# Performance work log

Measured on AMD Instinct MI355X. Metric: run time of the kernel, lower is better.

Reference implementation:

```python
import jax, jax.numpy as jnp
import numpy as np

D_MODEL = 1024
NUM_HEADS = 16
D_K = D_MODEL // NUM_HEADS


def setup_inputs() -> dict:
    key = jax.random.key(0)
    ks = jax.random.split(key, 9)
    B, S = 4, 2048
    scale = 1.0 / np.sqrt(D_MODEL)
    x = jax.random.normal(ks[0], (B, S, D_MODEL), dtype=jnp.float32)
    Wq = jax.random.uniform(ks[1], (D_MODEL, D_MODEL), jnp.float32, -scale, scale)
    Wk = jax.random.uniform(ks[2], (D_MODEL, D_MODEL), jnp.float32, -scale, scale)
    Wv = jax.random.uniform(ks[3], (D_MODEL, D_MODEL), jnp.float32, -scale, scale)
    Wo = jax.random.uniform(ks[4], (D_MODEL, D_MODEL), jnp.float32, -scale, scale)
    bq = jax.random.uniform(ks[5], (D_MODEL,), jnp.float32, -scale, scale)
    bk = jax.random.uniform(ks[6], (D_MODEL,), jnp.float32, -scale, scale)
    bv = jax.random.uniform(ks[7], (D_MODEL,), jnp.float32, -scale, scale)
    bo = jax.random.uniform(ks[8], (D_MODEL,), jnp.float32, -scale, scale)
    return {"x": x, "Wq": Wq, "bq": bq, "Wk": Wk, "bk": bk, "Wv": Wv, "bv": bv, "Wo": Wo, "bo": bo}


def _split_heads(t, B, S):
    # (B, S, D) -> (B, H, S, d_k)
    return t.reshape(B, S, NUM_HEADS, D_K).transpose(0, 2, 1, 3)


def reference(x, Wq, bq, Wk, bk, Wv, bv, Wo, bo):
    B, S, D = x.shape
    Q = _split_heads(x @ Wq + bq, B, S)
    K = _split_heads(x @ Wk + bk, B, S)
    V = _split_heads(x @ Wv + bv, B, S)
    # scores: (B, H, S, S) — naive materialization, faithful to original
    scores = jnp.einsum('bhqd,bhkd->bhqk', Q, K) / np.sqrt(D_K)
    weights = jax.nn.softmax(scores.astype(jnp.float32), axis=-1).astype(scores.dtype)
    # dropout p=0.0 in eval mode -> identity
    attn = jnp.einsum('bhqk,bhkd->bhqd', weights, V)
    attn = attn.transpose(0, 2, 1, 3).reshape(B, S, D)
    return attn @ Wo + bo
```

## Files before the change

kernel.cpp:

```cpp
#include <hip/hip_runtime.h>
#include <hip/hip_bf16.h>
#include <stdint.h>
#include <string.h>

using u16 = unsigned short;
typedef __attribute__((ext_vector_type(8))) short short8;
typedef __attribute__((ext_vector_type(4))) float f32x4;

__device__ __forceinline__ u16 f2bf(float f) {
  union { float f; unsigned int u; } x; x.f = f;
  unsigned int u = x.u;
  return (u16)((u + 0x7fffu + ((u >> 16) & 1u)) >> 16);
}
__device__ __forceinline__ unsigned int pk_bf16(float a, float b) {
  float2 t; t.x = a; t.y = b;
  __hip_bfloat162 h = __float22bfloat162_rn(t);
  unsigned int u; memcpy(&u, &h, 4);
  return u;
}
__device__ __forceinline__ void gl_lds16(const u16* g, u16* l) {
  __builtin_amdgcn_global_load_lds((const __attribute__((address_space(1))) void*)g,
                                   (__attribute__((address_space(3))) void*)l, 16, 0, 0);
}

__device__ __forceinline__ void pl_swap(unsigned int& a, unsigned int& b) {
  auto r1 = __builtin_amdgcn_permlane32_swap(a, b, false, false);
  auto r2 = __builtin_amdgcn_permlane16_swap(r1[0], r1[1], false, false);
  a = r2[0]; b = r2[1];
}

#define SCALE_LOG2E 0.18033688011112042f

__global__ void __launch_bounds__(256) conv_x(
    const float* __restrict__ in, u16* __restrict__ out, int n4) {
  const int t = blockIdx.x * 256 + threadIdx.x;
  if (t >= n4) return;
  const float4 v = ((const float4*)in)[t];
  uint2 o;
  o.x = pk_bf16(v.x, v.y);
  o.y = pk_bf16(v.z, v.w);
  ((uint2*)out)[t] = o;
}

__global__ void __launch_bounds__(256) transpose_w(
    const float* __restrict__ W0, const float* __restrict__ W1,
    const float* __restrict__ W2, const float* __restrict__ W3,
    u16* __restrict__ Wt) {
  __shared__ alignas(16) u16 t[64][65];
  const int z = blockIdx.z;
  const float* in = (z == 0) ? W0 : (z == 1) ? W1 : (z == 2) ? W2 : W3;
  u16* out = Wt + (size_t)z * 1024 * 1024;
  const int tx = threadIdx.x & 63, ty = threadIdx.x >> 6;
  const int r0 = blockIdx.y * 64, c0 = blockIdx.x * 64;
#pragma unroll
  for (int rr = ty; rr < 64; rr += 4) t[rr][tx] = f2bf(in[(size_t)(r0 + rr) * 1024 + c0 + tx]);
  __syncthreads();
#pragma unroll
  for (int rr = ty; rr < 64; rr += 4) out[(size_t)(c0 + rr) * 1024 + r0 + tx] = t[tx][rr];
}

__device__ __forceinline__ void gemm_core(
    const u16* __restrict__ A, const u16* __restrict__ Bt,
    u16* As, u16* Bs, int m0, int n0, int K, f32x4 (&acc)[4][4]) {
  const int tid = threadIdx.x;
  const int wave = tid >> 6, lane = tid & 63;
  const int quad = lane >> 4, l16 = lane & 15;
  const int wr = wave >> 1, wc = wave & 1;
  const int lr = lane >> 2, lc = (lane & 3) * 8;
  for (int k0 = 0; k0 < K; k0 += 32) {
    __syncthreads();
#pragma unroll
    for (int t = 0; t < 2; ++t) {
      const int c = wave + t * 4;
      gl_lds16(A  + (size_t)(m0 + c * 16 + lr) * K + k0 + lc, &As[c * 16 * 32]);
      gl_lds16(Bt + (size_t)(n0 + c * 16 + lr) * K + k0 + lc, &Bs[c * 16 * 32]);
    }
    __syncthreads();
    short8 af[4], bfr[4];
#pragma unroll
    for (int i = 0; i < 4; ++i)
      af[i] = *(const short8*)&As[(wr * 64 + i * 16 + l16) * 32 + quad * 8];
#pragma unroll
    for (int j = 0; j < 4; ++j)
      bfr[j] = *(const short8*)&Bs[(wc * 64 + j * 16 + l16) * 32 + quad * 8];
#pragma unroll
    for (int i = 0; i < 4; ++i)
#pragma unroll
      for (int j = 0; j < 4; ++j)
        acc[i][j] = __builtin_amdgcn_mfma_f32_16x16x32_bf16(af[i], bfr[j], acc[i][j], 0, 0, 0);
  }
}

__global__ void __launch_bounds__(256) gemm_qkv(
    const u16* __restrict__ A, const u16* __restrict__ Wt,
    const float* __restrict__ bq, const float* __restrict__ bk, const float* __restrict__ bv,
    u16* __restrict__ Qb, u16* __restrict__ Kb, u16* __restrict__ Vtb) {
  __shared__ alignas(16) u16 As[128 * 32];
  __shared__ alignas(16) u16 Bs[128 * 32];
  const int tsel = blockIdx.x >> 3;
  const int n0 = (blockIdx.x & 7) * 128;
  const int m0 = blockIdx.y * 128;
  const u16* Bt = Wt + (size_t)tsel * 1048576;
  const float* bias = (tsel == 0) ? bq : (tsel == 1) ? bk : bv;

  f32x4 acc[4][4];
#pragma unroll
  for (int i = 0; i < 4; ++i)
#pragma unroll
    for (int j = 0; j < 4; ++j) acc[i][j] = (f32x4){0.f, 0.f, 0.f, 0.f};

  gemm_core(A, Bt, As, Bs, m0, n0, 1024, acc);

  const int tid = threadIdx.x;
  const int wave = tid >> 6, lane = tid & 63;
  const int quad = lane >> 4, l16 = lane & 15;
  const int wr = wave >> 1, wc = wave & 1;

  if (tsel < 2) {
    u16* C = tsel ? Kb : Qb;
    const float scl = tsel ? 1.0f : SCALE_LOG2E;
#pragma unroll
    for (int j = 0; j < 4; ++j) {
      const int n = n0 + wc * 64 + j * 16 + l16;
      const float bvf = bias[n];
      const int h = n >> 6, d = n & 63;
#pragma unroll
      for (int i = 0; i < 4; ++i) {
        const int mbase = m0 + wr * 64 + i * 16 + quad * 4;
#pragma unroll
        for (int r = 0; r < 4; ++r) {
          const int m = mbase + r;
          const int b = m >> 11, s = m & 2047;
          C[((((size_t)b * 16 + h) * 2048) + s) * 64 + d] = f2bf((acc[i][j][r] + bvf) * scl);
        }
      }
    }
  } else {
#pragma unroll
    for (int j = 0; j < 4; ++j) {
      const int n = n0 + wc * 64 + j * 16 + l16;
      const float bvf = bias[n];
      const int h = n >> 6, d = n & 63;
#pragma unroll
      for (int i = 0; i < 4; ++i) {
        const int mbase = m0 + wr * 64 + i * 16 + quad * 4;
        const int b = mbase >> 11, s = mbase & 2047;
        uint2 o;
        o.x = pk_bf16(acc[i][j][0] + bvf, acc[i][j][1] + bvf);
        o.y = pk_bf16(acc[i][j][2] + bvf, acc[i][j][3] + bvf);
        *(uint2*)&Vtb[(((size_t)b * 16 + h) * 64 + d) * 2048 + s] = o;
      }
    }
  }
}

__global__ void __launch_bounds__(256) gemm_out(
    const u16* __restrict__ A, const u16* __restrict__ Bt,
    const float* __restrict__ bias, float* __restrict__ C, int N) {
  __shared__ alignas(16) u16 As[128 * 32];
  __shared__ alignas(16) u16 Bs[128 * 32];
  const int m0 = blockIdx.y * 128;
  const int n0 = blockIdx.x * 128;
  f32x4 acc[4][4];
#pragma unroll
  for (int i = 0; i < 4; ++i)
#pragma unroll
    for (int j = 0; j < 4; ++j) acc[i][j] = (f32x4){0.f, 0.f, 0.f, 0.f};

  gemm_core(A, Bt, As, Bs, m0, n0, 1024, acc);

  const int tid = threadIdx.x;
  const int wave = tid >> 6, lane = tid & 63;
  const int quad = lane >> 4, l16 = lane & 15;
  const int wr = wave >> 1, wc = wave & 1;
#pragma unroll
  for (int j = 0; j < 4; ++j) {
    const int n = n0 + wc * 64 + j * 16 + l16;
    const float bvf = bias[n];
#pragma unroll
    for (int i = 0; i < 4; ++i) {
      const int mbase = m0 + wr * 64 + i * 16 + quad * 4;
#pragma unroll
      for (int r = 0; r < 4; ++r)
        C[(size_t)(mbase + r) * N + n] = acc[i][j][r] + bvf;
    }
  }
}

__global__ void __launch_bounds__(256) flash_attn(
    const u16* __restrict__ Q, const u16* __restrict__ Kp,
    const u16* __restrict__ Vt, u16* __restrict__ Aout) {
  __shared__ alignas(16) u16 Qs[128 * 64];
  __shared__ alignas(16) u16 Ks[2][64 * 64];
  __shared__ alignas(16) u16 Vs[2][64 * 64];

  const int tid = threadIdx.x;
  const int wave = tid >> 6;
  const int lane = tid & 63;
  const int quad = lane >> 4;
  const int l16 = lane & 15;

  const int i = blockIdx.x;
  const int bh = (i & 7) * 8 + (i >> 7);
  const int q0 = ((i >> 3) & 15) * 128;
  const int b = bh >> 4, h = bh & 15;

  const u16* Qg = Q + (size_t)bh * 2048 * 64;
  const u16* Kg = Kp + (size_t)bh * 2048 * 64;
  const u16* Vg = Vt + (size_t)bh * 64 * 2048;

  const int lr8 = lane >> 3;
  const int cbg = ((lane & 7) ^ lr8) * 8;

#pragma unroll
  for (int t = 0; t < 4; ++t) {
    const int c = wave * 4 + t;
    gl_lds16(Qg + (size_t)(q0 + c * 8 + lr8) * 64 + cbg, &Qs[c * 8 * 64]);
  }
  {
#pragma unroll
    for (int t = 0; t < 2; ++t) {
      const int c = wave * 2 + t;
      gl_lds16(Kg + (size_t)(c * 8 + lr8) * 64 + cbg, &Ks[0][c * 8 * 64]);
      gl_lds16(Vg + (size_t)(c * 8 + lr8) * 2048 + cbg, &Vs[0][c * 8 * 64]);
    }
  }

  f32x4 oacc[2][4];
#pragma unroll
  for (int qb = 0; qb < 2; ++qb)
#pragma unroll
    for (int t = 0; t < 4; ++t) oacc[qb][t] = (f32x4){0.f, 0.f, 0.f, 0.f};
  f32x4 lacc[2];
  lacc[0] = (f32x4){0.f, 0.f, 0.f, 0.f};
  lacc[1] = (f32x4){0.f, 0.f, 0.f, 0.f};
  const int sw = (l16 & 7) * 8;

  short8 ones;
#pragma unroll
  for (int i2 = 0; i2 < 8; ++i2) ones[i2] = (short)0x3F80;

  __syncthreads();
  short8 qf[2][2];
#pragma unroll
  for (int qb = 0; qb < 2; ++qb)
#pragma unroll
    for (int ks = 0; ks < 2; ++ks)
      qf[qb][ks] = *(const short8*)&Qs[(wave * 32 + qb * 16 + l16) * 64 + (((ks * 4 + quad) * 8) ^ sw)];

  for (int kt = 0; kt < 32; ++kt) {
    const int p = kt & 1;
    if (kt + 1 < 32) {
      const int s1 = (kt + 1) * 64;
#pragma unroll
      for (int t = 0; t < 2; ++t) {
        const int c = wave * 2 + t;
        gl_lds16(Kg + (size_t)(s1 + c * 8 + lr8) * 64 + cbg, &Ks[p ^ 1][c * 8 * 64]);
        gl_lds16(Vg + (size_t)(c * 8 + lr8) * 2048 + s1 + cbg, &Vs[p ^ 1][c * 8 * 64]);
      }
    }
    const u16* Kc = &Ks[p][0];
    const u16* Vc = &Vs[p][0];

    f32x4 sacc[2][4];
#pragma unroll
    for (int qb = 0; qb < 2; ++qb)
#pragma unroll
      for (int t = 0; t < 4; ++t) sacc[qb][t] = (f32x4){0.f, 0.f, 0.f, 0.f};
#pragma unroll
    for (int ks = 0; ks < 2; ++ks) {
#pragma unroll
      for (int t = 0; t < 4; ++t) {
        const short8 akf = *(const short8*)&Kc[(t * 16 + l16) * 64 + (((ks * 4 + quad) * 8) ^ sw)];
#pragma unroll
        for (int qb = 0; qb < 2; ++qb)
          sacc[qb][t] = __builtin_amdgcn_mfma_f32_16x16x32_bf16(akf, qf[qb][ks], sacc[qb][t], 0, 0, 0);
      }
    }

    short8 bpf[2][2];
#pragma unroll
    for (int qb = 0; qb < 2; ++qb) {
      unsigned int w[4][2];
#pragma unroll
      for (int t = 0; t < 4; ++t) {
        const float p0 = __builtin_amdgcn_exp2f(sacc[qb][t][0]);
        const float p1 = __builtin_amdgcn_exp2f(sacc[qb][t][1]);
        const float p2 = __builtin_amdgcn_exp2f(sacc[qb][t][2]);
        const float p3 = __builtin_amdgcn_exp2f(sacc[qb][t][3]);
        w[t][0] = pk_bf16(p0, p1);
        w[t][1] = pk_bf16(p2, p3);
      }
      pl_swap(w[0][0], w[1][0]);
      pl_swap(w[0][1], w[1][1]);
      pl_swap(w[2][0], w[3][0]);
      pl_swap(w[2][1], w[3][1]);
      union { short8 s8; unsigned int u[4]; } pb;
      pb.u[0] = w[0][0]; pb.u[1] = w[0][1]; pb.u[2] = w[1][0]; pb.u[3] = w[1][1];
      bpf[qb][0] = pb.s8;
      pb.u[0] = w[2][0]; pb.u[1] = w[2][1]; pb.u[2] = w[3][0]; pb.u[3] = w[3][1];
      bpf[qb][1] = pb.s8;
    }

#pragma unroll
    for (int s = 0; s < 2; ++s)
#pragma unroll
      for (int qb = 0; qb < 2; ++qb)
        lacc[qb] = __builtin_amdgcn_mfma_f32_16x16x32_bf16(ones, bpf[qb][s], lacc[qb], 0, 0, 0);

#pragma unroll
    for (int s = 0; s < 2; ++s) {
#pragma unroll
      for (int t = 0; t < 4; ++t) {
        const short8 avf = *(const short8*)&Vc[(t * 16 + l16) * 64 + (((s * 4 + quad) * 8) ^ sw)];
#pragma unroll
        for (int qb = 0; qb < 2; ++qb)
          oacc[qb][t] = __builtin_amdgcn_mfma_f32_16x16x32_bf16(avf, bpf[qb][s], oacc[qb][t], 0, 0, 0);
      }
    }

    __syncthreads();
  }

#pragma unroll
  for (int qb = 0; qb < 2; ++qb) {
    const float inv = 1.0f / lacc[qb][0];
    const int qrow = q0 + wave * 32 + qb * 16 + l16;
    const size_t base = ((size_t)b * 2048 + qrow) * 1024 + h * 64 + quad * 4;
#pragma unroll
    for (int t = 0; t < 4; ++t) {
      uint2 o;
      o.x = pk_bf16(oacc[qb][t][0] * inv, oacc[qb][t][1] * inv);
      o.y = pk_bf16(oacc[qb][t][2] * inv, oacc[qb][t][3] * inv);
      *(uint2*)&Aout[base + t * 16] = o;
    }
  }
}

extern "C" void kernel_launch(void* const* d_in, const int* in_sizes, int n_in,
                              void* d_out, int out_size, void* d_ws, size_t ws_size,
                              hipStream_t stream) {
  (void)in_sizes; (void)n_in; (void)out_size; (void)ws_size;
  const float* x  = (const float*)d_in[0];
  const float* Wq = (const float*)d_in[1];
  const float* bq = (const float*)d_in[2];
  const float* Wk = (const float*)d_in[3];
  const float* bk = (const float*)d_in[4];
  const float* Wv = (const float*)d_in[5];
  const float* bv = (const float*)d_in[6];
  const float* Wo = (const float*)d_in[7];
  const float* bo = (const float*)d_in[8];
  float* out = (float*)d_out;

  u16* ws = (u16*)d_ws;
  const size_t SZ = (size_t)4 * 16 * 2048 * 64;
  u16* xb   = ws;
  u16* Qb   = ws + SZ;
  u16* Kb   = ws + 2 * SZ;
  u16* Vtb  = ws + 3 * SZ;
  u16* Wt   = ws + 4 * SZ;
  u16* Attn = ws;

  dim3 blk(256);
  conv_x<<<dim3(8192), blk, 0, stream>>>(x, xb, 2097152);
  transpose_w<<<dim3(16, 16, 4), blk, 0, stream>>>(Wq, Wk, Wv, Wo, Wt);
  gemm_qkv<<<dim3(24, 64), blk, 0, stream>>>(xb, Wt, bq, bk, bv, Qb, Kb, Vtb);
  flash_attn<<<dim3(1024), blk, 0, stream>>>(Qb, Kb, Vtb, Attn);
  gemm_out<<<dim3(8, 64), blk, 0, stream>>>(Attn, Wt + (size_t)3 * 1048576, bo, out, 1024);
}
```

Before: 316.0 us.

## Rewrite projection GEMMs as 256x128 tiles with double-buffered swizzled LDS pipeline

Replaces the simple 128x128, K=32 GEMM core with a 256x128 tile per 512-thread block. It uses K=64 steps, XOR-swizzled LDS layout and double-buffered global-to-LDS loads that are staggered across two MFMA phases, plus s_setprio around the MFMA bursts. The aim is to hide global load latency, avoid LDS bank conflicts and raise data reuse per block. The cost is higher LDS use (96KB per block), more register pressure and fewer blocks (768 and 256), which may underfill the GPU.

```diff
diff --git a/kernel.cpp b/kernel.cpp
--- a/kernel.cpp
+++ b/kernel.cpp
@@ -59,47 +59,114 @@
   for (int rr = ty; rr < 64; rr += 4) out[(size_t)(c0 + rr) * 1024 + r0 + tx] = t[tx][rr];
 }
 
-__device__ __forceinline__ void gemm_core(
+__device__ __forceinline__ void gemm256_core(
     const u16* __restrict__ A, const u16* __restrict__ Bt,
-    u16* As, u16* Bs, int m0, int n0, int K, f32x4 (&acc)[4][4]) {
+    u16 (*As)[16384], u16 (*Bs)[8192],
+    int m0, int n0, int K, f32x4 (&acc)[4][4]) {
   const int tid = threadIdx.x;
   const int wave = tid >> 6, lane = tid & 63;
   const int quad = lane >> 4, l16 = lane & 15;
-  const int wr = wave >> 1, wc = wave & 1;
-  const int lr = lane >> 2, lc = (lane & 3) * 8;
-  for (int k0 = 0; k0 < K; k0 += 32) {
-    __syncthreads();
-#pragma unroll
-    for (int t = 0; t < 2; ++t) {
-      const int c = wave + t * 4;
-      gl_lds16(A  + (size_t)(m0 + c * 16 + lr) * K + k0 + lc, &As[c * 16 * 32]);
-      gl_lds16(Bt + (size_t)(n0 + c * 16 + lr) * K + k0 + lc, &Bs[c * 16 * 32]);
-    }
-    __syncthreads();
-    short8 af[4], bfr[4];
+  const int wm = wave >> 1, wn = wave & 1;
+  const int lr8 = lane >> 3;
+  const int cbg = ((lane & 7) ^ lr8) * 8;
+  const int NT = K >> 6;
+
+  const int arow = wm * 64 + l16;
+  const int brow = wn * 64 + l16;
+  int kx[2];
+  kx[0] = ((quad    ) ^ (l16 & 7)) * 8;
+  kx[1] = ((quad + 4) ^ (l16 & 7)) * 8;
+
+#pragma unroll
+  for (int u = 0; u < 4; ++u)
+    gl_lds16(A + (size_t)(m0 + u * 64 + wave * 8 + lr8) * K + cbg,
+             &As[0][u * 4096 + wave * 512]);
+#pragma unroll
+  for (int v = 0; v < 2; ++v)
+    gl_lds16(Bt + (size_t)(n0 + v * 64 + wave * 8 + lr8) * K + cbg,
+             &Bs[0][v * 4096 + wave * 512]);
+#pragma unroll
+  for (int u = 0; u < 3; ++u)
+    gl_lds16(A + (size_t)(m0 + u * 64 + wave * 8 + lr8) * K + 64 + cbg,
+             &As[1][u * 4096 + wave * 512]);
+  asm volatile("s_waitcnt vmcnt(3)" ::: "memory");
+  __builtin_amdgcn_s_barrier();
+
+  for (int t = 0; t < NT; ++t) {
+    const int p = t & 1;
+    const u16* Ap = As[p];
+    const u16* Bp = Bs[p];
+
+    short8 af[4][2], bf[2][2];
 #pragma unroll
     for (int i = 0; i < 4; ++i)
-      af[i] = *(const short8*)&As[(wr * 64 + i * 16 + l16) * 32 + quad * 8];
-#pragma unroll
-    for (int j = 0; j < 4; ++j)
-      bfr[j] = *(const short8*)&Bs[(wc * 64 + j * 16 + l16) * 32 + quad * 8];
-#pragma unroll
-    for (int i = 0; i < 4; ++i)
-#pragma unroll
-      for (int j = 0; j < 4; ++j)
-        acc[i][j] = __builtin_amdgcn_mfma_f32_16x16x32_bf16(af[i], bfr[j], acc[i][j], 0, 0, 0);
-  }
-}
-
-__global__ void __launch_bounds__(256) gemm_qkv(
+#pragma unroll
+      for (int ks = 0; ks < 2; ++ks)
+        af[i][ks] = *(const short8*)&Ap[(arow + i * 16) * 64 + kx[ks]];
+#pragma unroll
+    for (int j = 0; j < 2; ++j)
+#pragma unroll
+      for (int ks = 0; ks < 2; ++ks)
+        bf[j][ks] = *(const short8*)&Bp[(brow + j * 16) * 64 + kx[ks]];
+    if (t + 1 < NT) {
+      gl_lds16(A + (size_t)(m0 + 3 * 64 + wave * 8 + lr8) * K + (t + 1) * 64 + cbg,
+               &As[p ^ 1][3 * 4096 + wave * 512]);
+      gl_lds16(Bt + (size_t)(n0 + wave * 8 + lr8) * K + (t + 1) * 64 + cbg,
+               &Bs[p ^ 1][wave * 512]);
+      gl_lds16(Bt + (size_t)(n0 + 64 + wave * 8 + lr8) * K + (t + 1) * 64 + cbg,
+               &Bs[p ^ 1][4096 + wave * 512]);
+    }
+    __builtin_amdgcn_s_barrier();
+    __builtin_amdgcn_s_setprio(1);
+#pragma unroll
+    for (int ks = 0; ks < 2; ++ks)
+#pragma unroll
+      for (int i = 0; i < 4; ++i)
+#pragma unroll
+        for (int j = 0; j < 2; ++j)
+          acc[i][j] = __builtin_amdgcn_mfma_f32_16x16x32_bf16(af[i][ks], bf[j][ks], acc[i][j], 0, 0, 0);
+    __builtin_amdgcn_s_setprio(0);
+    __builtin_amdgcn_s_barrier();
+
+#pragma unroll
+    for (int j = 0; j < 2; ++j)
+#pragma unroll
+      for (int ks = 0; ks < 2; ++ks)
+        bf[j][ks] = *(const short8*)&Bp[(brow + (j + 2) * 16) * 64 + kx[ks]];
+    if (t + 2 < NT) {
+#pragma unroll
+      for (int u = 0; u < 3; ++u)
+        gl_lds16(A + (size_t)(m0 + u * 64 + wave * 8 + lr8) * K + (t + 2) * 64 + cbg,
+                 &As[p][u * 4096 + wave * 512]);
+    }
+    __builtin_amdgcn_s_barrier();
+    __builtin_amdgcn_s_setprio(1);
+#pragma unroll
+    for (int ks = 0; ks < 2; ++ks)
+#pragma unroll
+      for (int i = 0; i < 4; ++i)
+#pragma unroll
+        for (int j = 0; j < 2; ++j)
+          acc[i][j + 2] = __builtin_amdgcn_mfma_f32_16x16x32_bf16(af[i][ks], bf[j][ks], acc[i][j + 2], 0, 0, 0);
+    __builtin_amdgcn_s_setprio(0);
+    if (t + 2 < NT) {
+      asm volatile("s_waitcnt vmcnt(3)" ::: "memory");
+    } else {
+      asm volatile("s_waitcnt vmcnt(0)" ::: "memory");
+    }
+    __builtin_amdgcn_s_barrier();
+  }
+}
+
+__global__ void __launch_bounds__(512, 2) gemm_qkv(
     const u16* __restrict__ A, const u16* __restrict__ Wt,
     const float* __restrict__ bq, const float* __restrict__ bk, const float* __restrict__ bv,
     u16* __restrict__ Qb, u16* __restrict__ Kb, u16* __restrict__ Vtb) {
-  __shared__ alignas(16) u16 As[128 * 32];
-  __shared__ alignas(16) u16 Bs[128 * 32];
+  __shared__ alignas(16) u16 As[2][16384];
+  __shared__ alignas(16) u16 Bs[2][8192];
   const int tsel = blockIdx.x >> 3;
   const int n0 = (blockIdx.x & 7) * 128;
-  const int m0 = blockIdx.y * 128;
+  const int m0 = blockIdx.y * 256;
   const u16* Bt = Wt + (size_t)tsel * 1048576;
   const float* bias = (tsel == 0) ? bq : (tsel == 1) ? bk : bv;
 
@@ -109,24 +176,24 @@
 #pragma unroll
     for (int j = 0; j < 4; ++j) acc[i][j] = (f32x4){0.f, 0.f, 0.f, 0.f};
 
-  gemm_core(A, Bt, As, Bs, m0, n0, 1024, acc);
+  gemm256_core(A, Bt, As, Bs, m0, n0, 1024, acc);
 
   const int tid = threadIdx.x;
   const int wave = tid >> 6, lane = tid & 63;
   const int quad = lane >> 4, l16 = lane & 15;
-  const int wr = wave >> 1, wc = wave & 1;
+  const int wm = wave >> 1, wn = wave & 1;
 
   if (tsel < 2) {
     u16* C = tsel ? Kb : Qb;
     const float scl = tsel ? 1.0f : SCALE_LOG2E;
 #pragma unroll
     for (int j = 0; j < 4; ++j) {
-      const int n = n0 + wc * 64 + j * 16 + l16;
+      const int n = n0 + wn * 64 + j * 16 + l16;
       const float bvf = bias[n];
       const int h = n >> 6, d = n & 63;
 #pragma unroll
       for (int i = 0; i < 4; ++i) {
-        const int mbase = m0 + wr * 64 + i * 16 + quad * 4;
+        const int mbase = m0 + wm * 64 + i * 16 + quad * 4;
 #pragma unroll
         for (int r = 0; r < 4; ++r) {
           const int m = mbase + r;
@@ -138,12 +205,12 @@
   } else {
 #pragma unroll
     for (int j = 0; j < 4; ++j) {
-      const int n = n0 + wc * 64 + j * 16 + l16;
+      const int n = n0 + wn * 64 + j * 16 + l16;
       const float bvf = bias[n];
       const int h = n >> 6, d = n & 63;
 #pragma unroll
       for (int i = 0; i < 4; ++i) {
-        const int mbase = m0 + wr * 64 + i * 16 + quad * 4;
+        const int mbase = m0 + wm * 64 + i * 16 + quad * 4;
         const int b = mbase >> 11, s = mbase & 2047;
         uint2 o;
         o.x = pk_bf16(acc[i][j][0] + bvf, acc[i][j][1] + bvf);
@@ -154,12 +221,12 @@
   }
 }
 
-__global__ void __launch_bounds__(256) gemm_out(
+__global__ void __launch_bounds__(512, 2) gemm_out(
     const u16* __restrict__ A, const u16* __restrict__ Bt,
     const float* __restrict__ bias, float* __restrict__ C, int N) {
-  __shared__ alignas(16) u16 As[128 * 32];
-  __shared__ alignas(16) u16 Bs[128 * 32];
-  const int m0 = blockIdx.y * 128;
+  __shared__ alignas(16) u16 As[2][16384];
+  __shared__ alignas(16) u16 Bs[2][8192];
+  const int m0 = blockIdx.y * 256;
   const int n0 = blockIdx.x * 128;
   f32x4 acc[4][4];
 #pragma unroll
@@ -167,19 +234,19 @@
 #pragma unroll
     for (int j = 0; j < 4; ++j) acc[i][j] = (f32x4){0.f, 0.f, 0.f, 0.f};
 
-  gemm_core(A, Bt, As, Bs, m0, n0, 1024, acc);
+  gemm256_core(A, Bt, As, Bs, m0, n0, 1024, acc);
 
   const int tid = threadIdx.x;
   const int wave = tid >> 6, lane = tid & 63;
   const int quad = lane >> 4, l16 = lane & 15;
-  const int wr = wave >> 1, wc = wave & 1;
+  const int wm = wave >> 1, wn = wave & 1;
 #pragma unroll
   for (int j = 0; j < 4; ++j) {
-    const int n = n0 + wc * 64 + j * 16 + l16;
+    const int n = n0 + wn * 64 + j * 16 + l16;
     const float bvf = bias[n];
 #pragma unroll
     for (int i = 0; i < 4; ++i) {
-      const int mbase = m0 + wr * 64 + i * 16 + quad * 4;
+      const int mbase = m0 + wm * 64 + i * 16 + quad * 4;
 #pragma unroll
       for (int r = 0; r < 4; ++r)
         C[(size_t)(mbase + r) * N + n] = acc[i][j][r] + bvf;
@@ -361,10 +428,9 @@
   u16* Wt   = ws + 4 * SZ;
   u16* Attn = ws;
 
-  dim3 blk(256);
-  conv_x<<<dim3(8192), blk, 0, stream>>>(x, xb, 2097152);
-  transpose_w<<<dim3(16, 16, 4), blk, 0, stream>>>(Wq, Wk, Wv, Wo, Wt);
-  gemm_qkv<<<dim3(24, 64), blk, 0, stream>>>(xb, Wt, bq, bk, bv, Qb, Kb, Vtb);
-  flash_attn<<<dim3(1024), blk, 0, stream>>>(Qb, Kb, Vtb, Attn);
-  gemm_out<<<dim3(8, 64), blk, 0, stream>>>(Attn, Wt + (size_t)3 * 1048576, bo, out, 1024);
-}
+  conv_x<<<dim3(8192), dim3(256), 0, stream>>>(x, xb, 2097152);
+  transpose_w<<<dim3(16, 16, 4), dim3(256), 0, stream>>>(Wq, Wk, Wv, Wo, Wt);
+  gemm_qkv<<<dim3(24, 32), dim3(512), 0, stream>>>(xb, Wt, bq, bk, bv, Qb, Kb, Vtb);
+  flash_attn<<<dim3(1024), dim3(256), 0, stream>>>(Qb, Kb, Vtb, Attn);
+  gemm_out<<<dim3(8, 32), dim3(512), 0, stream>>>(Attn, Wt + (size_t)3 * 1048576, bo, out, 1024);
+}
```

New measurement: 316.4 us. No clear change (+0.1%).

## Double GEMM k-tile to 64 with XOR-swizzled LDS layout

Applied to the files above, without the earlier changes.

The shared GEMM core now stages 64-wide k-slices per iteration instead of 32, which halves the number of barrier pairs. It stores rows in LDS with an XOR swizzle on the 16-byte chunk index so the MFMA fragment reads avoid bank conflicts. LDS use per block doubles to 32 KB, which may lower occupancy. The launch code is only cosmetically rewritten.

```diff
diff --git a/kernel.cpp b/kernel.cpp
--- a/kernel.cpp
+++ b/kernel.cpp
@@ -66,28 +66,35 @@
   const int wave = tid >> 6, lane = tid & 63;
   const int quad = lane >> 4, l16 = lane & 15;
   const int wr = wave >> 1, wc = wave & 1;
-  const int lr = lane >> 2, lc = (lane & 3) * 8;
-  for (int k0 = 0; k0 < K; k0 += 32) {
+  const int lr8 = lane >> 3;
+  const int cbg = ((lane & 7) ^ lr8) * 8;
+  const int sw = (l16 & 7);
+  for (int k0 = 0; k0 < K; k0 += 64) {
     __syncthreads();
 #pragma unroll
-    for (int t = 0; t < 2; ++t) {
-      const int c = wave + t * 4;
-      gl_lds16(A  + (size_t)(m0 + c * 16 + lr) * K + k0 + lc, &As[c * 16 * 32]);
-      gl_lds16(Bt + (size_t)(n0 + c * 16 + lr) * K + k0 + lc, &Bs[c * 16 * 32]);
+    for (int u = 0; u < 4; ++u) {
+      gl_lds16(A  + (size_t)(m0 + u * 32 + wave * 8 + lr8) * K + k0 + cbg,
+               &As[u * 2048 + wave * 512]);
+      gl_lds16(Bt + (size_t)(n0 + u * 32 + wave * 8 + lr8) * K + k0 + cbg,
+               &Bs[u * 2048 + wave * 512]);
     }
     __syncthreads();
-    short8 af[4], bfr[4];
-#pragma unroll
-    for (int i = 0; i < 4; ++i)
-      af[i] = *(const short8*)&As[(wr * 64 + i * 16 + l16) * 32 + quad * 8];
-#pragma unroll
-    for (int j = 0; j < 4; ++j)
-      bfr[j] = *(const short8*)&Bs[(wc * 64 + j * 16 + l16) * 32 + quad * 8];
-#pragma unroll
-    for (int i = 0; i < 4; ++i)
+#pragma unroll
+    for (int ks = 0; ks < 2; ++ks) {
+      const int kc = ((ks * 4 + quad) ^ sw) * 8;
+      short8 af[4], bfr[4];
+#pragma unroll
+      for (int i = 0; i < 4; ++i)
+        af[i] = *(const short8*)&As[(wr * 64 + i * 16 + l16) * 64 + kc];
 #pragma unroll
       for (int j = 0; j < 4; ++j)
-        acc[i][j] = __builtin_amdgcn_mfma_f32_16x16x32_bf16(af[i], bfr[j], acc[i][j], 0, 0, 0);
+        bfr[j] = *(const short8*)&Bs[(wc * 64 + j * 16 + l16) * 64 + kc];
+#pragma unroll
+      for (int i = 0; i < 4; ++i)
+#pragma unroll
+        for (int j = 0; j < 4; ++j)
+          acc[i][j] = __builtin_amdgcn_mfma_f32_16x16x32_bf16(af[i], bfr[j], acc[i][j], 0, 0, 0);
+    }
   }
 }
 
@@ -95,8 +102,8 @@
     const u16* __restrict__ A, const u16* __restrict__ Wt,
     const float* __restrict__ bq, const float* __restrict__ bk, const float* __restrict__ bv,
     u16* __restrict__ Qb, u16* __restrict__ Kb, u16* __restrict__ Vtb) {
-  __shared__ alignas(16) u16 As[128 * 32];
-  __shared__ alignas(16) u16 Bs[128 * 32];
+  __shared__ alignas(16) u16 As[128 * 64];
+  __shared__ alignas(16) u16 Bs[128 * 64];
   const int tsel = blockIdx.x >> 3;
   const int n0 = (blockIdx.x & 7) * 128;
   const int m0 = blockIdx.y * 128;
@@ -157,8 +164,8 @@
 __global__ void __launch_bounds__(256) gemm_out(
     const u16* __restrict__ A, const u16* __restrict__ Bt,
     const float* __restrict__ bias, float* __restrict__ C, int N) {
-  __shared__ alignas(16) u16 As[128 * 32];
-  __shared__ alignas(16) u16 Bs[128 * 32];
+  __shared__ alignas(16) u16 As[128 * 64];
+  __shared__ alignas(16) u16 Bs[128 * 64];
   const int m0 = blockIdx.y * 128;
   const int n0 = blockIdx.x * 128;
   f32x4 acc[4][4];
@@ -361,10 +368,9 @@
   u16* Wt   = ws + 4 * SZ;
   u16* Attn = ws;
 
-  dim3 blk(256);
-  conv_x<<<dim3(8192), blk, 0, stream>>>(x, xb, 2097152);
-  transpose_w<<<dim3(16, 16, 4), blk, 0, stream>>>(Wq, Wk, Wv, Wo, Wt);
-  gemm_qkv<<<dim3(24, 64), blk, 0, stream>>>(xb, Wt, bq, bk, bv, Qb, Kb, Vtb);
-  flash_attn<<<dim3(1024), blk, 0, stream>>>(Qb, Kb, Vtb, Attn);
-  gemm_out<<<dim3(8, 64), blk, 0, stream>>>(Attn, Wt + (size_t)3 * 1048576, bo, out, 1024);
-}
+  conv_x<<<dim3(8192), dim3(256), 0, stream>>>(x, xb, 2097152);
+  transpose_w<<<dim3(16, 16, 4), dim3(256), 0, stream>>>(Wq, Wk, Wv, Wo, Wt);
+  gemm_qkv<<<dim3(24, 64), dim3(256), 0, stream>>>(xb, Wt, bq, bk, bv, Qb, Kb, Vtb);
+  flash_attn<<<dim3(1024), dim3(256), 0, stream>>>(Qb, Kb, Vtb, Attn);
+  gemm_out<<<dim3(8, 64), dim3(256), 0, stream>>>(Attn, Wt + (size_t)3 * 1048576, bo, out, 1024);
+}
```

Result: faster. 308.9 us (-2.3%).
